# Performance work log

Measured on AMD Instinct MI355X. Metric: run time of the kernel, lower is better.

## Reference

```python
import jax, jax.numpy as jnp
import numpy as np

BEAM = 4


def _gru_step(x_emb, h, W_ih, W_hh, b_ih, b_hh):
    gi = x_emb @ W_ih + b_ih
    gh = h @ W_hh + b_hh
    ir, iz, ig = jnp.split(gi, 3, axis=-1)
    hr, hz, hg = jnp.split(gh, 3, axis=-1)
    r = jax.nn.sigmoid(ir + hr)
    z = jax.nn.sigmoid(iz + hz)
    n = jnp.tanh(ig + r * hg)
    return (1.0 - z) * n + z * h


def _beam_search(xs, E, W_ih, W_hh, b_ih, b_hh, W_out, b_out, maxtime, beamsize):
    B = xs.shape[0]
    K = beamsize
    H = W_hh.shape[0]
    T = maxtime + 1  # torch loop runs for t in range(maxtime + 1)

    x0 = jnp.broadcast_to(xs[None, :], (K, B))          # all beams start from same ids
    h0 = jnp.zeros((K, B, H), E.dtype)                  # initial cell state (per beam)
    scores0 = jnp.zeros((B, K), E.dtype)
    seqs0 = jnp.zeros((B, K, T), jnp.int32)

    def step(carry, t):
        x_t, h, beam_scores, seqs = carry
        xf = x_t.reshape(K * B)
        hf = h.reshape(K * B, H)
        h_new = _gru_step(E[xf], hf, W_ih, W_hh, b_ih, b_hh)      # [K*B, H]
        logp = jax.nn.log_softmax(h_new @ W_out + b_out, axis=-1)  # [K*B, V]
        # per-beam top-k candidates (torch: sort descending, take first beamsize)
        top_s, top_x = jax.lax.top_k(logp, K)                      # [K*B, K]
        top_s = top_s.reshape(K, B, K)
        top_x = top_x.reshape(K, B, K)
        # trans[b, from, to] = beam_scores[b, from] + top_s[from, b, to]
        trans = beam_scores[:, :, None] + jnp.transpose(top_s, (1, 0, 2))
        trans_f = trans.reshape(B, K * K)
        order = jnp.argsort(-trans_f, axis=-1)[:, :K]              # [B, K] flat indices
        bfrom = order // K                                          # source beam
        new_scores = jnp.take_along_axis(trans_f, order, axis=-1)  # [B, K]
        xs_f = jnp.transpose(top_x, (1, 0, 2)).reshape(B, K * K)
        new_x = jnp.take_along_axis(xs_f, order, axis=-1)          # [B, K] new symbols
        # gather cell states from source beams
        h_b = jnp.transpose(h_new.reshape(K, B, H), (1, 0, 2))     # [B, K, H]
        h_g = jnp.take_along_axis(h_b, bfrom[:, :, None], axis=1)  # [B, K, H]
        h_next = jnp.transpose(h_g, (1, 0, 2))                     # [K, B, H]
        # gather sequences from source beams and append new symbol at position t
        seqs = jnp.take_along_axis(seqs, bfrom[:, :, None], axis=1)
        seqs = jax.lax.dynamic_update_index_in_dim(seqs, new_x, t, axis=2)
        return (new_x.T, h_next, new_scores, seqs), None

    (_, _, scoresT, seqsT), _ = jax.lax.scan(
        step, (x0, h0, scores0, seqs0), jnp.arange(T))
    return seqsT, scoresT


def setup_inputs() -> dict:
    key = jax.random.key(0)
    ks = jax.random.split(key, 5)
    B, D, H, V = 64, 512, 512, 50257
    return {
        "xs": jax.random.randint(ks[0], (B,), 0, V, dtype=jnp.int32),
        "E": jax.random.normal(ks[1], (V, D), jnp.float32) * 0.02,
        "W_ih": jax.random.normal(ks[2], (D, 3 * H), jnp.float32) * 0.02,
        "W_hh": jax.random.normal(ks[3], (H, 3 * H), jnp.float32) * 0.02,
        "b_ih": jnp.zeros((3 * H,), jnp.float32),
        "b_hh": jnp.zeros((3 * H,), jnp.float32),
        "W_out": jax.random.normal(ks[4], (H, V), jnp.float32) * 0.02,
        "b_out": jnp.zeros((V,), jnp.float32),
        "maxtime": 15,
    }


def reference(xs, E, W_ih, W_hh, b_ih, b_hh, W_out, b_out, maxtime):
    seqs, _ = _beam_search(xs, E, W_ih, W_hh, b_ih, b_hh, W_out, b_out,
                           maxtime, beamsize=BEAM)
    # torch returns beam_seqs[0] (the top-scoring beam) stacked -> [batch, T]
    return seqs[:, 0, :]
```

## Files before the change

kernel.cpp:

```cpp
#include <hip/hip_runtime.h>
#include <math.h>

#define BB 64
#define KK 4
#define RR 256
#define DD 512
#define HH 512
#define T3 1536
#define VV 50257
#define NSTR 393

struct SRec {
  float v[4];
  int   ix[4];
  float ms;
  float pad;
  double S;
};

__global__ __launch_bounds__(256) void k_init(const int* __restrict__ xs,
                                              float* __restrict__ hCur,
                                              float* __restrict__ scores,
                                              int* __restrict__ curx) {
  int i = blockIdx.x * 256 + threadIdx.x;
  if (i < HH * RR) hCur[i] = 0.0f;
  if (i < RR) {
    scores[i] = 0.0f;
    curx[i] = xs[i & 63];
  }
}

__global__ __launch_bounds__(256) void k_gru(const float* __restrict__ Etab,
                                             const float* __restrict__ Wih,
                                             const float* __restrict__ Whh,
                                             const float* __restrict__ bih,
                                             const float* __restrict__ bhh,
                                             const float* __restrict__ hCur,
                                             float* __restrict__ hStage,
                                             const int* __restrict__ curx) {
  const int tid = threadIdx.x;
  const int jloc = tid & 7;
  const int bg = tid >> 3;
  const int j = blockIdx.x * 8 + jloc;
  const int rowbase = blockIdx.y * 64;
  const int b0 = bg * 2;

  __shared__ float xe[64 * 33];
  __shared__ float hp[64 * 33];
  __shared__ int xl[64];
  if (tid < 64) xl[tid] = curx[rowbase + tid];

  float a[12];
#pragma unroll
  for (int i = 0; i < 12; ++i) a[i] = 0.0f;

  for (int kt = 0; kt < 16; ++kt) {
    __syncthreads();
    const int kb = kt * 32;
#pragma unroll
    for (int i = 0; i < 8; ++i) {
      int idx = i * 256 + tid;
      int b = idx >> 5, kk = idx & 31;
      xe[b * 33 + kk] = Etab[(size_t)xl[b] * DD + kb + kk];
    }
#pragma unroll
    for (int i = 0; i < 8; ++i) {
      int idx = i * 256 + tid;
      int kk = idx >> 6, bl = idx & 63;
      hp[bl * 33 + kk] = hCur[(size_t)(kb + kk) * RR + rowbase + bl];
    }
    __syncthreads();
#pragma unroll 4
    for (int kk = 0; kk < 32; ++kk) {
      const size_t krow = (size_t)(kb + kk) * T3;
      float wir = Wih[krow + j];
      float wiz = Wih[krow + j + HH];
      float wig = Wih[krow + j + 2 * HH];
      float whr = Whh[krow + j];
      float whz = Whh[krow + j + HH];
      float whg = Whh[krow + j + 2 * HH];
      float x0v = xe[b0 * 33 + kk];
      float x1v = xe[(b0 + 1) * 33 + kk];
      float h0v = hp[b0 * 33 + kk];
      float h1v = hp[(b0 + 1) * 33 + kk];
      a[0] += x0v * wir; a[1]  += x0v * wiz; a[2]  += x0v * wig;
      a[3] += h0v * whr; a[4]  += h0v * whz; a[5]  += h0v * whg;
      a[6] += x1v * wir; a[7]  += x1v * wiz; a[8]  += x1v * wig;
      a[9] += h1v * whr; a[10] += h1v * whz; a[11] += h1v * whg;
    }
  }

  const float bir = bih[j], biz = bih[HH + j], big = bih[2 * HH + j];
  const float bhr = bhh[j], bhz = bhh[HH + j], bhg = bhh[2 * HH + j];
#pragma unroll
  for (int p = 0; p < 2; ++p) {
    const int row = rowbase + b0 + p;
    float ir = a[6 * p + 0] + bir;
    float iz = a[6 * p + 1] + biz;
    float ig = a[6 * p + 2] + big;
    float hr = a[6 * p + 3] + bhr;
    float hz = a[6 * p + 4] + bhz;
    float hg = a[6 * p + 5] + bhg;
    float r = 1.0f / (1.0f + expf(-(ir + hr)));
    float z = 1.0f / (1.0f + expf(-(iz + hz)));
    float n = tanhf(ig + r * hg);
    float hprev = hCur[(size_t)j * RR + row];
    hStage[(size_t)j * RR + row] = (1.0f - z) * n + z * hprev;
  }
}

__device__ __forceinline__ void merge44(float* v, int* ix, const float* ov, const int* oix) {
  float rv[4]; int rix[4];
  int a = 0, b = 0;
#pragma unroll
  for (int t = 0; t < 4; ++t) {
    bool ta;
    if (a >= 4) ta = false;
    else if (b >= 4) ta = true;
    else ta = (v[a] > ov[b]) || (v[a] == ov[b] && ix[a] < oix[b]);
    if (ta) { rv[t] = v[a]; rix[t] = ix[a]; ++a; }
    else    { rv[t] = ov[b]; rix[t] = oix[b]; ++b; }
  }
#pragma unroll
  for (int t = 0; t < 4; ++t) { v[t] = rv[t]; ix[t] = rix[t]; }
}

__global__ __launch_bounds__(256) void k_logits(const float* __restrict__ Wout,
                                                const float* __restrict__ bout,
                                                const float* __restrict__ hStage,
                                                SRec* __restrict__ sbuf) {
  const int n = blockIdx.x;
  const int cls = n & 7;
  const int m = n >> 3;
  const int s = cls + 8 * (m >> 3);
  const int y = m & 7;
  if (s >= NSTR) return;

  const int tid = threadIdx.x;
  const int wid = tid >> 6;
  const int ct = tid & 63;
  const int scol = s * 128;
  const int c0 = scol + ct;
  const bool okA = (c0 < VV);
  const bool okB = (c0 + 64 < VV);
  const int cA = okA ? c0 : (VV - 1);
  const int cB = okB ? (c0 + 64) : (VV - 1);
  const int rowU = __builtin_amdgcn_readfirstlane(y * 32 + wid * 8);

  const float* __restrict__ WA = Wout + cA;
  const float* __restrict__ WB = Wout + cB;

  float acc[8][2];
#pragma unroll
  for (int ri = 0; ri < 8; ++ri) { acc[ri][0] = 0.0f; acc[ri][1] = 0.0f; }

  float wA0[8], wB0[8], wA1[8], wB1[8];

  auto loadW = [&](float* wA, float* wB, int kb) {
#pragma unroll
    for (int i = 0; i < 8; ++i) {
      wA[i] = WA[(size_t)(kb + i) * VV];
      wB[i] = WB[(size_t)(kb + i) * VV];
    }
  };
  auto fmaC = [&](const float* wA, const float* wB, int kb) {
#pragma unroll
    for (int i = 0; i < 8; ++i) {
      const float4* hg = reinterpret_cast<const float4*>(
          hStage + (size_t)(kb + i) * RR + rowU);
      float4 h0 = hg[0], h1 = hg[1];
      float hr[8] = {h0.x, h0.y, h0.z, h0.w, h1.x, h1.y, h1.z, h1.w};
#pragma unroll
      for (int ri = 0; ri < 8; ++ri) {
        acc[ri][0] += hr[ri] * wA[i];
        acc[ri][1] += hr[ri] * wB[i];
      }
    }
  };

  loadW(wA0, wB0, 0);
  for (int c = 0; c < 64; c += 2) {
    loadW(wA1, wB1, (c + 1) * 8);
    fmaC(wA0, wB0, c * 8);
    if (c + 2 < 64) loadW(wA0, wB0, (c + 2) * 8);
    fmaC(wA1, wB1, (c + 1) * 8);
  }

  const float boA = bout[cA];
  const float boB = bout[cB];
#pragma unroll
  for (int ri = 0; ri < 8; ++ri) {
    float vA = okA ? (acc[ri][0] + boA) : -INFINITY;
    float vB = okB ? (acc[ri][1] + boB) : -INFINITY;
    float v[4]; int ix[4];
    if (vB > vA) { v[0] = vB; ix[0] = c0 + 64; v[1] = vA; ix[1] = okA ? c0 : 0x7fffffff; }
    else         { v[0] = vA; ix[0] = okA ? c0 : 0x7fffffff; v[1] = vB; ix[1] = okB ? (c0 + 64) : 0x7fffffff; }
    v[2] = -INFINITY; ix[2] = 0x7fffffff;
    v[3] = -INFINITY; ix[3] = 0x7fffffff;
#pragma unroll
    for (int mm = 1; mm < 64; mm <<= 1) {
      float ov[4]; int oix[4];
#pragma unroll
      for (int jj = 0; jj < 4; ++jj) {
        ov[jj] = __shfl_xor(v[jj], mm, 64);
        oix[jj] = __shfl_xor(ix[jj], mm, 64);
      }
      merge44(v, ix, ov, oix);
    }
    const float ms = v[0];
    double sl = 0.0;
    if (okA) sl += (double)expf(vA - ms);
    if (okB) sl += (double)expf(vB - ms);
#pragma unroll
    for (int mm = 1; mm < 64; mm <<= 1) sl += __shfl_xor(sl, mm, 64);
    if (ct == 0) {
      const int row = rowU + ri;
      SRec* rec = &sbuf[(size_t)row * NSTR + s];
#pragma unroll
      for (int jj = 0; jj < 4; ++jj) { rec->v[jj] = v[jj]; rec->ix[jj] = ix[jj]; }
      rec->ms = ms;
      rec->S = sl;
    }
  }
}

__device__ inline void merge84(float* v, int* ix, const float* ov, const int* oix) {
  float rv[8]; int rix[8];
  int a = 0, b = 0;
#pragma unroll
  for (int t = 0; t < 8; ++t) {
    bool ta;
    if (a >= 8) ta = false;
    else if (b >= 4) ta = true;
    else ta = (v[a] > ov[b]) || (v[a] == ov[b] && ix[a] < oix[b]);
    if (ta) { rv[t] = v[a]; rix[t] = ix[a]; ++a; }
    else    { rv[t] = ov[b]; rix[t] = oix[b]; ++b; }
  }
#pragma unroll
  for (int t = 0; t < 8; ++t) { v[t] = rv[t]; ix[t] = rix[t]; }
}

__device__ inline void merge88(float* v, int* ix, const float* ov, const int* oix) {
  float rv[8]; int rix[8];
  int a = 0, b = 0;
#pragma unroll
  for (int t = 0; t < 8; ++t) {
    bool ta;
    if (a >= 8) ta = false;
    else if (b >= 8) ta = true;
    else ta = (v[a] > ov[b]) || (v[a] == ov[b] && ix[a] < oix[b]);
    if (ta) { rv[t] = v[a]; rix[t] = ix[a]; ++a; }
    else    { rv[t] = ov[b]; rix[t] = oix[b]; ++b; }
  }
#pragma unroll
  for (int t = 0; t < 8; ++t) { v[t] = rv[t]; ix[t] = rix[t]; }
}

__global__ __launch_bounds__(64) void k_merge(const SRec* __restrict__ sbuf,
                                              float* __restrict__ topq,
                                              int* __restrict__ topi) {
  const int row = blockIdx.x;
  const int l = threadIdx.x;
  float lv[8]; int li[8];
#pragma unroll
  for (int jj = 0; jj < 8; ++jj) { lv[jj] = -INFINITY; li[jj] = 0x7fffffff; }
  float lms[7]; double lS[7];
  int ns = 0;
  for (int s = l; s < NSTR; s += 64) {
    const SRec* rec = &sbuf[(size_t)row * NSTR + s];
    float mv[4]; int mi[4];
#pragma unroll
    for (int jj = 0; jj < 4; ++jj) { mv[jj] = rec->v[jj]; mi[jj] = rec->ix[jj]; }
    lms[ns] = rec->ms;
    lS[ns] = rec->S;
    ++ns;
    merge84(lv, li, mv, mi);
  }
#pragma unroll
  for (int m = 1; m < 64; m <<= 1) {
    float ov[8]; int oi[8];
#pragma unroll
    for (int jj = 0; jj < 8; ++jj) {
      ov[jj] = __shfl_xor(lv[jj], m, 64);
      oi[jj] = __shfl_xor(li[jj], m, 64);
    }
    merge88(lv, li, ov, oi);
  }
  const float mg = lv[0];
  double Z = 0.0;
  for (int i = 0; i < ns; ++i) Z += lS[i] * (double)expf(lms[i] - mg);
#pragma unroll
  for (int m = 1; m < 64; m <<= 1) Z += __shfl_xor(Z, m, 64);
  const float Zf = (float)Z;
  const float L32 = (float)log((double)Zf);
  float q[8];
#pragma unroll
  for (int jj = 0; jj < 8; ++jj) {
    float g = lv[jj] - mg;
    q[jj] = g - L32;
  }
  float sq[8]; int si[8];
#pragma unroll
  for (int jj = 0; jj < 8; ++jj) {
    float cv = q[jj]; int ci = li[jj];
    int pos = jj;
    for (int kk2 = 0; kk2 < jj; ++kk2) {
      if (cv > sq[kk2] || (cv == sq[kk2] && ci < si[kk2])) { pos = kk2; break; }
    }
    for (int kk2 = jj; kk2 > pos; --kk2) { sq[kk2] = sq[kk2 - 1]; si[kk2] = si[kk2 - 1]; }
    sq[pos] = cv; si[pos] = ci;
  }
  if (l == 0) {
#pragma unroll
    for (int jj = 0; jj < 4; ++jj) {
      topq[row * 4 + jj] = sq[jj];
      topi[row * 4 + jj] = si[jj];
    }
  }
}

__global__ __launch_bounds__(64) void k_beam(const float* __restrict__ topq,
                                             const int* __restrict__ topi,
                                             float* __restrict__ scores,
                                             int* __restrict__ curx,
                                             int* __restrict__ bfrom) {
  const int b = threadIdx.x;
  float sc[4];
#pragma unroll
  for (int f = 0; f < 4; ++f) sc[f] = scores[f * 64 + b];
  float tv[16];
#pragma unroll
  for (int f = 0; f < 4; ++f)
#pragma unroll
    for (int to = 0; to < 4; ++to)
      tv[f * 4 + to] = sc[f] + topq[(f * 64 + b) * 4 + to];

  float ov[4]; int ord[4]; int cnt = 0;
#pragma unroll
  for (int flat = 0; flat < 16; ++flat) {
    float v = tv[flat];
    int pos = -1;
    for (int j = 0; j < cnt; ++j)
      if (v > ov[j]) { pos = j; break; }
    if (pos < 0) {
      if (cnt < 4) { ov[cnt] = v; ord[cnt] = flat; ++cnt; }
    } else {
      int last = (cnt < 4) ? cnt : 3;
      for (int j = last; j > pos; --j) { ov[j] = ov[j - 1]; ord[j] = ord[j - 1]; }
      ov[pos] = v; ord[pos] = flat;
      if (cnt < 4) ++cnt;
    }
  }
#pragma unroll
  for (int s = 0; s < 4; ++s) {
    int flat = ord[s];
    int f = flat >> 2, to = flat & 3;
    int tok = topi[(f * 64 + b) * 4 + to];
    scores[s * 64 + b] = ov[s];
    curx[s * 64 + b] = tok;
    bfrom[s * 64 + b] = f;
  }
}

__global__ __launch_bounds__(256) void k_hgather(const float* __restrict__ hStage,
                                                 float* __restrict__ hCur,
                                                 const int* __restrict__ bfrom) {
  int idx = blockIdx.x * 256 + threadIdx.x;
  int j = idx >> 8, r = idx & 255;
  int s = r >> 6, b = r & 63;
  hCur[(size_t)j * RR + r] = hStage[(size_t)j * RR + bfrom[s * 64 + b] * 64 + b];
}

__global__ __launch_bounds__(256) void k_seq(const int* __restrict__ src,
                                             int* __restrict__ dst,
                                             const int* __restrict__ bfrom,
                                             const int* __restrict__ curx,
                                             int t, int T) {
  int tid = threadIdx.x;
  int s = tid >> 6, b = tid & 63;
  int bf = bfrom[s * 64 + b];
  for (int u = 0; u < t; ++u)
    dst[(b * KK + s) * T + u] = src[(b * KK + bf) * T + u];
  dst[(b * KK + s) * T + t] = curx[s * 64 + b];
}

__global__ __launch_bounds__(256) void k_out(const int* __restrict__ seqs,
                                             int* __restrict__ outp, int T) {
  int idx = blockIdx.x * 256 + threadIdx.x;
  if (idx < BB * T) {
    int b = idx / T, u = idx % T;
    outp[b * T + u] = seqs[(b * KK + 0) * T + u];
  }
}

extern "C" void kernel_launch(void* const* d_in, const int* in_sizes, int n_in,
                              void* d_out, int out_size, void* d_ws, size_t ws_size,
                              hipStream_t stream) {
  (void)in_sizes; (void)n_in; (void)ws_size;
  const int* xs = (const int*)d_in[0];
  const float* Etab = (const float*)d_in[1];
  const float* Wih = (const float*)d_in[2];
  const float* Whh = (const float*)d_in[3];
  const float* bih = (const float*)d_in[4];
  const float* bhh = (const float*)d_in[5];
  const float* Wout = (const float*)d_in[6];
  const float* bout = (const float*)d_in[7];
  int* outp = (int*)d_out;
  const int T = out_size / BB;

  SRec* sbuf = (SRec*)d_ws;
  float* hCur = (float*)(sbuf + (size_t)RR * NSTR);
  float* hStage = hCur + (size_t)HH * RR;
  float* topq = hStage + (size_t)HH * RR;
  int* topi = (int*)(topq + RR * 4);
  float* scores = (float*)(topi + RR * 4);
  int* curx = (int*)(scores + RR);
  int* bfrom = curx + RR;
  int* seqA = bfrom + RR;
  int* seqB = seqA + BB * KK * T;

  k_init<<<dim3(512), dim3(256), 0, stream>>>(xs, hCur, scores, curx);
  for (int t = 0; t < T; ++t) {
    int* ssrc = (t % 2 == 0) ? seqA : seqB;
    int* sdst = (t % 2 == 0) ? seqB : seqA;
    k_gru<<<dim3(64, 4), dim3(256), 0, stream>>>(Etab, Wih, Whh, bih, bhh,
                                                 hCur, hStage, curx);
    k_logits<<<dim3(3200), dim3(256), 0, stream>>>(Wout, bout, hStage, sbuf);
    k_merge<<<dim3(RR), dim3(64), 0, stream>>>(sbuf, topq, topi);
    k_beam<<<dim3(1), dim3(64), 0, stream>>>(topq, topi, scores, curx, bfrom);
    k_hgather<<<dim3(512), dim3(256), 0, stream>>>(hStage, hCur, bfrom);
    k_seq<<<dim3(1), dim3(256), 0, stream>>>(ssrc, sdst, bfrom, curx, t, T);
  }
  int* sfin = (T % 2 == 0) ? seqA : seqB;
  k_out<<<dim3((BB * T + 255) / 256), dim3(256), 0, stream>>>(sfin, outp, T);
}
```

Before: 7.901 ms.

## Fuse beam gather into GRU, merge beam+seq kernels, vectorize Wout loads

The hidden-state gather by source beam now happens inside the GRU kernel's loads, with ping-pong h buffers, so the separate gather kernel and its copy are gone. The beam selection and sequence-copy kernels are merged into one launch. The logits kernel loads two adjacent Wout columns per lane as a float2 on all but the last strip and shuffles the results back to the original column assignment. This cuts launches per step and raises load width, at the cost of extra shuffles and indirect h loads.

Result: slower. 8.641 ms (+9.4%).

```diff
diff --git a/kernel.cpp b/kernel.cpp
--- a/kernel.cpp
+++ b/kernel.cpp
@@ -10,6 +10,8 @@
 #define VV 50257
 #define NSTR 393
 
+typedef float f2v __attribute__((ext_vector_type(2), aligned(4)));
+
 struct SRec {
   float v[4];
   int   ix[4];
@@ -19,14 +21,16 @@
 };
 
 __global__ __launch_bounds__(256) void k_init(const int* __restrict__ xs,
-                                              float* __restrict__ hCur,
+                                              float* __restrict__ hA,
                                               float* __restrict__ scores,
-                                              int* __restrict__ curx) {
+                                              int* __restrict__ curx,
+                                              int* __restrict__ bfrom) {
   int i = blockIdx.x * 256 + threadIdx.x;
-  if (i < HH * RR) hCur[i] = 0.0f;
+  if (i < HH * RR) hA[i] = 0.0f;
   if (i < RR) {
     scores[i] = 0.0f;
     curx[i] = xs[i & 63];
+    bfrom[i] = i >> 6;
   }
 }
 
@@ -35,9 +39,10 @@
                                              const float* __restrict__ Whh,
                                              const float* __restrict__ bih,
                                              const float* __restrict__ bhh,
-                                             const float* __restrict__ hCur,
-                                             float* __restrict__ hStage,
-                                             const int* __restrict__ curx) {
+                                             const float* __restrict__ hin,
+                                             float* __restrict__ hout,
+                                             const int* __restrict__ curx,
+                                             const int* __restrict__ bfrom) {
   const int tid = threadIdx.x;
   const int jloc = tid & 7;
   const int bg = tid >> 3;
@@ -48,7 +53,11 @@
   __shared__ float xe[64 * 33];
   __shared__ float hp[64 * 33];
   __shared__ int xl[64];
-  if (tid < 64) xl[tid] = curx[rowbase + tid];
+  __shared__ int bf[64];
+  if (tid < 64) {
+    xl[tid] = curx[rowbase + tid];
+    bf[tid] = bfrom[rowbase + tid];
+  }
 
   float a[12];
 #pragma unroll
@@ -67,7 +76,7 @@
     for (int i = 0; i < 8; ++i) {
       int idx = i * 256 + tid;
       int kk = idx >> 6, bl = idx & 63;
-      hp[bl * 33 + kk] = hCur[(size_t)(kb + kk) * RR + rowbase + bl];
+      hp[bl * 33 + kk] = hin[(size_t)(kb + kk) * RR + bf[bl] * 64 + bl];
     }
     __syncthreads();
 #pragma unroll 4
@@ -104,8 +113,8 @@
     float r = 1.0f / (1.0f + expf(-(ir + hr)));
     float z = 1.0f / (1.0f + expf(-(iz + hz)));
     float n = tanhf(ig + r * hg);
-    float hprev = hCur[(size_t)j * RR + row];
-    hStage[(size_t)j * RR + row] = (1.0f - z) * n + z * hprev;
+    float hprev = hin[(size_t)j * RR + bf[b0 + p] * 64 + (b0 + p)];
+    hout[(size_t)j * RR + row] = (1.0f - z) * n + z * hprev;
   }
 }
 
@@ -146,52 +155,102 @@
   const int cA = okA ? c0 : (VV - 1);
   const int cB = okB ? (c0 + 64) : (VV - 1);
   const int rowU = __builtin_amdgcn_readfirstlane(y * 32 + wid * 8);
-
-  const float* __restrict__ WA = Wout + cA;
-  const float* __restrict__ WB = Wout + cB;
+  const bool fast = (s < NSTR - 1);
 
   float acc[8][2];
 #pragma unroll
   for (int ri = 0; ri < 8; ++ri) { acc[ri][0] = 0.0f; acc[ri][1] = 0.0f; }
 
-  float wA0[8], wB0[8], wA1[8], wB1[8];
-
-  auto loadW = [&](float* wA, float* wB, int kb) {
-#pragma unroll
-    for (int i = 0; i < 8; ++i) {
-      wA[i] = WA[(size_t)(kb + i) * VV];
-      wB[i] = WB[(size_t)(kb + i) * VV];
-    }
-  };
-  auto fmaC = [&](const float* wA, const float* wB, int kb) {
-#pragma unroll
-    for (int i = 0; i < 8; ++i) {
-      const float4* hg = reinterpret_cast<const float4*>(
-          hStage + (size_t)(kb + i) * RR + rowU);
-      float4 h0 = hg[0], h1 = hg[1];
-      float hr[8] = {h0.x, h0.y, h0.z, h0.w, h1.x, h1.y, h1.z, h1.w};
-#pragma unroll
-      for (int ri = 0; ri < 8; ++ri) {
-        acc[ri][0] += hr[ri] * wA[i];
-        acc[ri][1] += hr[ri] * wB[i];
-      }
-    }
-  };
-
-  loadW(wA0, wB0, 0);
-  for (int c = 0; c < 64; c += 2) {
-    loadW(wA1, wB1, (c + 1) * 8);
-    fmaC(wA0, wB0, c * 8);
-    if (c + 2 < 64) loadW(wA0, wB0, (c + 2) * 8);
-    fmaC(wA1, wB1, (c + 1) * 8);
+  if (fast) {
+    const float* __restrict__ Wb = Wout + scol + 2 * ct;
+    float wE0[8], wO0[8], wE1[8], wO1[8];
+
+    auto loadW = [&](float* wE, float* wO, int kb) {
+#pragma unroll
+      for (int i = 0; i < 8; ++i) {
+        f2v t = *reinterpret_cast<const f2v*>(Wb + (size_t)(kb + i) * VV);
+        wE[i] = t.x; wO[i] = t.y;
+      }
+    };
+    auto fmaC = [&](const float* wE, const float* wO, int kb) {
+#pragma unroll
+      for (int i = 0; i < 8; ++i) {
+        const float4* hg = reinterpret_cast<const float4*>(
+            hStage + (size_t)(kb + i) * RR + rowU);
+        float4 h0 = hg[0], h1 = hg[1];
+        float hr[8] = {h0.x, h0.y, h0.z, h0.w, h1.x, h1.y, h1.z, h1.w};
+#pragma unroll
+        for (int ri = 0; ri < 8; ++ri) {
+          acc[ri][0] += hr[ri] * wE[i];
+          acc[ri][1] += hr[ri] * wO[i];
+        }
+      }
+    };
+
+    loadW(wE0, wO0, 0);
+    for (int c = 0; c < 64; c += 2) {
+      loadW(wE1, wO1, (c + 1) * 8);
+      fmaC(wE0, wO0, c * 8);
+      if (c + 2 < 64) loadW(wE0, wO0, (c + 2) * 8);
+      fmaC(wE1, wO1, (c + 1) * 8);
+    }
+  } else {
+    const float* __restrict__ WA = Wout + cA;
+    const float* __restrict__ WB = Wout + cB;
+    float wA0[8], wB0[8], wA1[8], wB1[8];
+
+    auto loadW = [&](float* wA, float* wB, int kb) {
+#pragma unroll
+      for (int i = 0; i < 8; ++i) {
+        wA[i] = WA[(size_t)(kb + i) * VV];
+        wB[i] = WB[(size_t)(kb + i) * VV];
+      }
+    };
+    auto fmaC = [&](const float* wA, const float* wB, int kb) {
+#pragma unroll
+      for (int i = 0; i < 8; ++i) {
+        const float4* hg = reinterpret_cast<const float4*>(
+            hStage + (size_t)(kb + i) * RR + rowU);
+        float4 h0 = hg[0], h1 = hg[1];
+        float hr[8] = {h0.x, h0.y, h0.z, h0.w, h1.x, h1.y, h1.z, h1.w};
+#pragma unroll
+        for (int ri = 0; ri < 8; ++ri) {
+          acc[ri][0] += hr[ri] * wA[i];
+          acc[ri][1] += hr[ri] * wB[i];
+        }
+      }
+    };
+
+    loadW(wA0, wB0, 0);
+    for (int c = 0; c < 64; c += 2) {
+      loadW(wA1, wB1, (c + 1) * 8);
+      fmaC(wA0, wB0, c * 8);
+      if (c + 2 < 64) loadW(wA0, wB0, (c + 2) * 8);
+      fmaC(wA1, wB1, (c + 1) * 8);
+    }
   }
 
   const float boA = bout[cA];
   const float boB = bout[cB];
+  const int srcLo = ct >> 1;
+  const int srcHi = 32 + (ct >> 1);
+  const bool odd = (ct & 1) != 0;
 #pragma unroll
   for (int ri = 0; ri < 8; ++ri) {
-    float vA = okA ? (acc[ri][0] + boA) : -INFINITY;
-    float vB = okB ? (acc[ri][1] + boB) : -INFINITY;
+    float aA, aB;
+    if (fast) {
+      float e  = __shfl(acc[ri][0], srcLo, 64);
+      float o  = __shfl(acc[ri][1], srcLo, 64);
+      aA = odd ? o : e;
+      float e2 = __shfl(acc[ri][0], srcHi, 64);
+      float o2 = __shfl(acc[ri][1], srcHi, 64);
+      aB = odd ? o2 : e2;
+    } else {
+      aA = acc[ri][0];
+      aB = acc[ri][1];
+    }
+    float vA = okA ? (aA + boA) : -INFINITY;
+    float vB = okB ? (aB + boB) : -INFINITY;
     float v[4]; int ix[4];
     if (vB > vA) { v[0] = vB; ix[0] = c0 + 64; v[1] = vA; ix[1] = okA ? c0 : 0x7fffffff; }
     else         { v[0] = vA; ix[0] = okA ? c0 : 0x7fffffff; v[1] = vB; ix[1] = okB ? (c0 + 64) : 0x7fffffff; }
@@ -319,69 +378,65 @@
   }
 }
 
-__global__ __launch_bounds__(64) void k_beam(const float* __restrict__ topq,
-                                             const int* __restrict__ topi,
-                                             float* __restrict__ scores,
-                                             int* __restrict__ curx,
-                                             int* __restrict__ bfrom) {
-  const int b = threadIdx.x;
-  float sc[4];
-#pragma unroll
-  for (int f = 0; f < 4; ++f) sc[f] = scores[f * 64 + b];
-  float tv[16];
-#pragma unroll
-  for (int f = 0; f < 4; ++f)
-#pragma unroll
-    for (int to = 0; to < 4; ++to)
-      tv[f * 4 + to] = sc[f] + topq[(f * 64 + b) * 4 + to];
-
-  float ov[4]; int ord[4]; int cnt = 0;
-#pragma unroll
-  for (int flat = 0; flat < 16; ++flat) {
-    float v = tv[flat];
-    int pos = -1;
-    for (int j = 0; j < cnt; ++j)
-      if (v > ov[j]) { pos = j; break; }
-    if (pos < 0) {
-      if (cnt < 4) { ov[cnt] = v; ord[cnt] = flat; ++cnt; }
-    } else {
-      int last = (cnt < 4) ? cnt : 3;
-      for (int j = last; j > pos; --j) { ov[j] = ov[j - 1]; ord[j] = ord[j - 1]; }
-      ov[pos] = v; ord[pos] = flat;
-      if (cnt < 4) ++cnt;
-    }
-  }
-#pragma unroll
-  for (int s = 0; s < 4; ++s) {
-    int flat = ord[s];
-    int f = flat >> 2, to = flat & 3;
-    int tok = topi[(f * 64 + b) * 4 + to];
-    scores[s * 64 + b] = ov[s];
-    curx[s * 64 + b] = tok;
-    bfrom[s * 64 + b] = f;
-  }
-}
-
-__global__ __launch_bounds__(256) void k_hgather(const float* __restrict__ hStage,
-                                                 float* __restrict__ hCur,
-                                                 const int* __restrict__ bfrom) {
-  int idx = blockIdx.x * 256 + threadIdx.x;
-  int j = idx >> 8, r = idx & 255;
-  int s = r >> 6, b = r & 63;
-  hCur[(size_t)j * RR + r] = hStage[(size_t)j * RR + bfrom[s * 64 + b] * 64 + b];
-}
-
-__global__ __launch_bounds__(256) void k_seq(const int* __restrict__ src,
-                                             int* __restrict__ dst,
-                                             const int* __restrict__ bfrom,
-                                             const int* __restrict__ curx,
-                                             int t, int T) {
-  int tid = threadIdx.x;
-  int s = tid >> 6, b = tid & 63;
-  int bf = bfrom[s * 64 + b];
+__global__ __launch_bounds__(256) void k_beamseq(const float* __restrict__ topq,
+                                                 const int* __restrict__ topi,
+                                                 float* __restrict__ scores,
+                                                 int* __restrict__ curx,
+                                                 int* __restrict__ bfrom,
+                                                 const int* __restrict__ src,
+                                                 int* __restrict__ dst,
+                                                 int t, int T) {
+  const int tid = threadIdx.x;
+  __shared__ int sh_bf[RR];
+  __shared__ int sh_cx[RR];
+
+  if (tid < 64) {
+    const int b = tid;
+    float sc[4];
+#pragma unroll
+    for (int f = 0; f < 4; ++f) sc[f] = scores[f * 64 + b];
+    float tv[16];
+#pragma unroll
+    for (int f = 0; f < 4; ++f)
+#pragma unroll
+      for (int to = 0; to < 4; ++to)
+        tv[f * 4 + to] = sc[f] + topq[(f * 64 + b) * 4 + to];
+
+    float ov[4]; int ord[4]; int cnt = 0;
+#pragma unroll
+    for (int flat = 0; flat < 16; ++flat) {
+      float v = tv[flat];
+      int pos = -1;
+      for (int j = 0; j < cnt; ++j)
+        if (v > ov[j]) { pos = j; break; }
+      if (pos < 0) {
+        if (cnt < 4) { ov[cnt] = v; ord[cnt] = flat; ++cnt; }
+      } else {
+        int last = (cnt < 4) ? cnt : 3;
+        for (int j = last; j > pos; --j) { ov[j] = ov[j - 1]; ord[j] = ord[j - 1]; }
+        ov[pos] = v; ord[pos] = flat;
+        if (cnt < 4) ++cnt;
+      }
+    }
+#pragma unroll
+    for (int s = 0; s < 4; ++s) {
+      int flat = ord[s];
+      int f = flat >> 2, to = flat & 3;
+      int tok = topi[(f * 64 + b) * 4 + to];
+      scores[s * 64 + b] = ov[s];
+      curx[s * 64 + b] = tok;
+      bfrom[s * 64 + b] = f;
+      sh_bf[s * 64 + b] = f;
+      sh_cx[s * 64 + b] = tok;
+    }
+  }
+  __syncthreads();
+
+  const int s2 = tid >> 6, b2 = tid & 63;
+  const int bf2 = sh_bf[s2 * 64 + b2];
   for (int u = 0; u < t; ++u)
-    dst[(b * KK + s) * T + u] = src[(b * KK + bf) * T + u];
-  dst[(b * KK + s) * T + t] = curx[s * 64 + b];
+    dst[(b2 * KK + s2) * T + u] = src[(b2 * KK + bf2) * T + u];
+  dst[(b2 * KK + s2) * T + t] = sh_cx[s2 * 64 + b2];
 }
 
 __global__ __launch_bounds__(256) void k_out(const int* __restrict__ seqs,
@@ -409,9 +464,9 @@
   const int T = out_size / BB;
 
   SRec* sbuf = (SRec*)d_ws;
-  float* hCur = (float*)(sbuf + (size_t)RR * NSTR);
-  float* hStage = hCur + (size_t)HH * RR;
-  float* topq = hStage + (size_t)HH * RR;
+  float* hA = (float*)(sbuf + (size_t)RR * NSTR);
+  float* hB = hA + (size_t)HH * RR;
+  float* topq = hB + (size_t)HH * RR;
   int* topi = (int*)(topq + RR * 4);
   float* scores = (float*)(topi + RR * 4);
   int* curx = (int*)(scores + RR);
@@ -419,17 +474,18 @@
   int* seqA = bfrom + RR;
   int* seqB = seqA + BB * KK * T;
 
-  k_init<<<dim3(512), dim3(256), 0, stream>>>(xs, hCur, scores, curx);
+  k_init<<<dim3(512), dim3(256), 0, stream>>>(xs, hA, scores, curx, bfrom);
   for (int t = 0; t < T; ++t) {
     int* ssrc = (t % 2 == 0) ? seqA : seqB;
     int* sdst = (t % 2 == 0) ? seqB : seqA;
+    float* hin = (t & 1) ? hB : hA;
+    float* hout = (t & 1) ? hA : hB;
     k_gru<<<dim3(64, 4), dim3(256), 0, stream>>>(Etab, Wih, Whh, bih, bhh,
-                                                 hCur, hStage, curx);
-    k_logits<<<dim3(3200), dim3(256), 0, stream>>>(Wout, bout, hStage, sbuf);
+                                                 hin, hout, curx, bfrom);
+    k_logits<<<dim3(3200), dim3(256), 0, stream>>>(Wout, bout, hout, sbuf);
     k_merge<<<dim3(RR), dim3(64), 0, stream>>>(sbuf, topq, topi);
-    k_beam<<<dim3(1), dim3(64), 0, stream>>>(topq, topi, scores, curx, bfrom);
-    k_hgather<<<dim3(512), dim3(256), 0, stream>>>(hStage, hCur, bfrom);
-    k_seq<<<dim3(1), dim3(256), 0, stream>>>(ssrc, sdst, bfrom, curx, t, T);
+    k_beamseq<<<dim3(1), dim3(256), 0, stream>>>(topq, topi, scores, curx,
+                                                 bfrom, ssrc, sdst, t, T);
   }
   int* sfin = (T % 2 == 0) ? seqA : seqB;
   k_out<<<dim3((BB * T + 255) / 256), dim3(256), 0, stream>>>(sfin, outp, T);
```
